# Optimization experiments

Measured on AMD Instinct MI355X. Metric: run time of the kernel, lower is better.

The kernel has to match this reference:

```python
import jax, jax.numpy as jnp
import numpy as np

W = 256  # window size


def _stack_neighbors(x):
    """x: (b, c, w, h, d) -> (b, c, w, h, d, 3): [prev chunk, self, next chunk],
    zero-padded at sequence boundaries (matches F.pad with value=0 in Longformer)."""
    prev = jnp.pad(x[:, :-1], ((0, 0), (1, 0), (0, 0), (0, 0), (0, 0)))
    nxt = jnp.pad(x[:, 1:], ((0, 0), (0, 1), (0, 0), (0, 0), (0, 0)))
    return jnp.stack([prev, x, nxt], axis=-1)


def setup_inputs() -> dict:
    key = jax.random.key(0)
    kq, kk, kv = jax.random.split(key, 3)
    b, s, h, d = 2, 8192, 8, 64
    return {
        "query": jax.random.normal(kq, (b, s, h, d), dtype=jnp.float32),
        "key": jax.random.normal(kk, (b, s, h, d), dtype=jnp.float32),
        "value": jax.random.normal(kv, (b, s, h, d), dtype=jnp.float32),
    }


def reference(query, key, value):
    b, s, h, d = query.shape
    c = s // W
    # --- sliding_chunks_no_overlap_matmul_qk ---
    chunk_q = query.reshape(b, c, W, h, d)
    chunk_k = key.reshape(b, c, W, h, d)
    k_exp = _stack_neighbors(chunk_k)            # (b, c, W, h, d, 3)
    # (b, c, W_q, h, 3, W_k)
    diag = jnp.einsum('bcxhd,bcyhde->bcxhey', chunk_q, k_exp)
    attention = diag.reshape(b, s, h, 3 * W)
    # softmax over the 3*W window positions (dropout = identity in eval)
    attention = jax.nn.softmax(attention, axis=-1)
    # --- sliding_chunks_no_overlap_matmul_pv ---
    chunk_prob = attention.reshape(b, c, W, h, 3, W)
    chunk_v = value.reshape(b, c, W, h, d)
    v_exp = _stack_neighbors(chunk_v)            # (b, c, W, h, d, 3)
    context = jnp.einsum('bcwhpd,bcdhep->bcwhe', chunk_prob, v_exp)
    output = context.reshape(b, s, h, d)
    return output, attention
```

## Files before the change

### kernel.cpp

```cpp
#include <hip/hip_runtime.h>


#define SEQ  8192
#define NH   8
#define DM   64
#define WIN  256
#define NC   32

typedef float  f32x4  __attribute__((ext_vector_type(4)));
typedef short  bf16x8 __attribute__((ext_vector_type(8)));
typedef short  bf16x4 __attribute__((ext_vector_type(4)));
typedef unsigned short u16;

__device__ __forceinline__ u16 bf16_rne(float x) {
    unsigned u = __builtin_bit_cast(unsigned, x);
    u += 0x7FFFu + ((u >> 16) & 1u);
    return (u16)(u >> 16);
}
__device__ __forceinline__ float bf16_f32(u16 h) {
    unsigned u = ((unsigned)h) << 16;
    return __builtin_bit_cast(float, u);
}

__global__ __launch_bounds__(256)
void wattn_prep(const float* __restrict__ kg, const float* __restrict__ vg,
                u16* __restrict__ khp, u16* __restrict__ klp, u16* __restrict__ vtp)
{
    __shared__ float tile[64 * 68];
    const int bid = blockIdx.x;
    const int t   = threadIdx.x;

    if (bid < 4096) {
        const size_t base = (size_t)bid * 2048 + t * 8;
        f32x4 a0 = *(const f32x4*)(kg + base);
        f32x4 a1 = *(const f32x4*)(kg + base + 4);
        bf16x8 h, l;
        #pragma unroll
        for (int i = 0; i < 8; ++i) {
            float f = (i < 4) ? a0[i] : a1[i - 4];
            u16 hh = bf16_rne(f);
            h[i] = (short)hh;
            l[i] = (short)bf16_rne(f - bf16_f32(hh));
        }
        *(bf16x8*)(khp + base) = h;
        *(bf16x8*)(klp + base) = l;
    } else {
        const int vid = bid - 4096;
        const int st  = vid & 127;
        const int hh  = (vid >> 7) & 7;
        const int bb  = vid >> 10;
        const int s0  = st * 64;

        const int r  = t >> 2;
        const int dg = (t & 3) * 16;
        const float* vp = vg + (((size_t)bb * SEQ + s0 + r) * NH + hh) * DM + dg;
        #pragma unroll
        for (int i = 0; i < 4; ++i)
            *(f32x4*)&tile[r * 68 + dg + 4 * i] = *(const f32x4*)(vp + 4 * i);
        __syncthreads();

        const int d  = t >> 2;
        const int sg = (t & 3) * 16;
        u16* op = vtp + (((size_t)bb * NH + hh) * DM + d) * SEQ + s0 + sg;
        bf16x8 o0, o1;
        #pragma unroll
        for (int j = 0; j < 8; ++j) o0[j] = (short)bf16_rne(tile[(sg + j) * 68 + d]);
        #pragma unroll
        for (int j = 0; j < 8; ++j) o1[j] = (short)bf16_rne(tile[(sg + 8 + j) * 68 + d]);
        *(bf16x8*)op       = o0;
        *(bf16x8*)(op + 8) = o1;
    }
}

__global__ __launch_bounds__(256, 2)
void wattn_mfma2(const float* __restrict__ qg, const u16* __restrict__ khp,
                 const u16* __restrict__ klp, const u16* __restrict__ vtp,
                 float* __restrict__ outg, float* __restrict__ attng)
{
    __shared__ __align__(16) char lds[35840];

    const int t    = threadIdx.x;
    const int lane = t & 63;
    const int w    = t >> 6;
    const int a    = lane & 15;
    const int g4   = lane >> 4;

    u16*   pw   = (u16*)(lds) + w * 2304;
    float* csc  = (float*)lds;
    float* smax = (float*)(lds + 34816);
    float* ssum = smax + 128;

    int gid = blockIdx.x;
    gid = (gid & 7) * 512 + (gid >> 3);
    const int tile = gid & 7;  gid >>= 3;
    const int hh   = gid & 7;  gid >>= 3;
    const int cc   = gid & 31; gid >>= 5;
    const int bb   = gid;
    const int row0 = cc * WIN + tile * 32;

    bf16x8 qh[2][2], ql[2][2];
    #pragma unroll
    for (int rt = 0; rt < 2; ++rt)
      #pragma unroll
      for (int ks = 0; ks < 2; ++ks) {
        const float* qp = qg + (((size_t)bb * SEQ + row0 + rt*16 + a) * NH + hh) * DM
                             + ks*32 + g4*8;
        f32x4 t0 = *(const f32x4*)qp;
        f32x4 t1 = *(const f32x4*)(qp + 4);
        #pragma unroll
        for (int i = 0; i < 8; ++i) {
            float f = (i < 4) ? t0[i] : t1[i - 4];
            u16 hv = bf16_rne(f);
            qh[rt][ks][i] = (short)hv;
            ql[rt][ks][i] = (short)bf16_rne(f - bf16_f32(hv));
        }
      }

    f32x4 acc[3][4][2];
    #pragma unroll
    for (int e = 0; e < 3; ++e)
      #pragma unroll
      for (int ct = 0; ct < 4; ++ct)
        #pragma unroll
        for (int rt = 0; rt < 2; ++rt)
            acc[e][ct][rt] = (f32x4){0.f, 0.f, 0.f, 0.f};

    #pragma unroll
    for (int e = 0; e < 3; ++e) {
        const int cs = cc + e - 1;
        if ((unsigned)cs < NC) {
            #pragma unroll
            for (int ct = 0; ct < 4; ++ct) {
                const size_t koff = (((size_t)bb * SEQ + cs*WIN + w*64 + ct*16 + a) * NH + hh) * DM
                                  + g4*8;
                #pragma unroll
                for (int ks = 0; ks < 2; ++ks) {
                    bf16x8 kh = *(const bf16x8*)(khp + koff + ks*32);
                    bf16x8 kl = *(const bf16x8*)(klp + koff + ks*32);
                    #pragma unroll
                    for (int rt = 0; rt < 2; ++rt) {
                        acc[e][ct][rt] = __builtin_amdgcn_mfma_f32_16x16x32_bf16(kh, qh[rt][ks], acc[e][ct][rt], 0, 0, 0);
                        acc[e][ct][rt] = __builtin_amdgcn_mfma_f32_16x16x32_bf16(kh, ql[rt][ks], acc[e][ct][rt], 0, 0, 0);
                        acc[e][ct][rt] = __builtin_amdgcn_mfma_f32_16x16x32_bf16(kl, qh[rt][ks], acc[e][ct][rt], 0, 0, 0);
                    }
                }
            }
        }
    }

    float M[2], INV[2];
    #pragma unroll
    for (int rt = 0; rt < 2; ++rt) {
        float mm = 0.f;
        #pragma unroll
        for (int e = 0; e < 3; ++e)
          #pragma unroll
          for (int ct = 0; ct < 4; ++ct)
            #pragma unroll
            for (int reg = 0; reg < 4; ++reg)
              mm = fmaxf(mm, acc[e][ct][rt][reg]);
        mm = fmaxf(mm, __shfl_xor(mm, 16));
        mm = fmaxf(mm, __shfl_xor(mm, 32));
        if (g4 == 0) smax[(rt*16 + a)*4 + w] = mm;
    }
    __syncthreads();
    #pragma unroll
    for (int rt = 0; rt < 2; ++rt) {
        const float* sp = smax + (rt*16 + a)*4;
        float mm = fmaxf(fmaxf(sp[0], sp[1]), fmaxf(sp[2], sp[3]));
        M[rt] = mm;
        float s = 0.f;
        #pragma unroll
        for (int e = 0; e < 3; ++e)
          #pragma unroll
          for (int ct = 0; ct < 4; ++ct)
            #pragma unroll
            for (int reg = 0; reg < 4; ++reg) {
                float p = __expf(acc[e][ct][rt][reg] - mm);
                acc[e][ct][rt][reg] = p;
                s += p;
            }
        s += __shfl_xor(s, 16);
        s += __shfl_xor(s, 32);
        if (g4 == 0) ssum[(rt*16 + a)*4 + w] = s;
    }
    __syncthreads();
    #pragma unroll
    for (int rt = 0; rt < 2; ++rt) {
        const float* sp = ssum + (rt*16 + a)*4;
        INV[rt] = 1.0f / (sp[0] + sp[1] + sp[2] + sp[3]);
    }

    #pragma unroll
    for (int rt = 0; rt < 2; ++rt) {
        float* ab = attng + (((size_t)bb * SEQ + row0 + rt*16 + a) * NH + hh) * 768
                          + w*64 + g4*4;
        #pragma unroll
        for (int e = 0; e < 3; ++e)
          #pragma unroll
          for (int ct = 0; ct < 4; ++ct) {
            f32x4 p = acc[e][ct][rt] * INV[rt];
            acc[e][ct][rt] = p;
            __builtin_nontemporal_store(p, (f32x4*)(ab + e*256 + ct*16));
          }
    }

    f32x4 acc2[4][2];
    #pragma unroll
    for (int dt = 0; dt < 4; ++dt)
      #pragma unroll
      for (int rt = 0; rt < 2; ++rt)
        acc2[dt][rt] = (f32x4){0.f, 0.f, 0.f, 0.f};

    #pragma unroll
    for (int e = 0; e < 3; ++e) {
        const int cs = cc + e - 1;
        if ((unsigned)cs < NC) {
            #pragma unroll
            for (int rt = 0; rt < 2; ++rt)
              #pragma unroll
              for (int ct = 0; ct < 4; ++ct) {
                f32x4 p = acc[e][ct][rt];
                bf16x4 pk;
                #pragma unroll
                for (int reg = 0; reg < 4; ++reg) pk[reg] = (short)bf16_rne(p[reg]);
                *(bf16x4*)(pw + (rt*16 + a)*72 + ct*16 + g4*4) = pk;
              }
            #pragma unroll
            for (int ks = 0; ks < 2; ++ks) {
                bf16x8 pb[2], va[4];
                #pragma unroll
                for (int rt = 0; rt < 2; ++rt)
                    pb[rt] = *(const bf16x8*)(pw + (rt*16 + a)*72 + ks*32 + g4*8);
                #pragma unroll
                for (int dt = 0; dt < 4; ++dt)
                    va[dt] = *(const bf16x8*)(vtp
                        + (((size_t)bb * NH + hh) * DM + dt*16 + a) * SEQ
                        + cs*WIN + w*64 + ks*32 + g4*8);
                #pragma unroll
                for (int dt = 0; dt < 4; ++dt)
                  #pragma unroll
                  for (int rt = 0; rt < 2; ++rt)
                    acc2[dt][rt] = __builtin_amdgcn_mfma_f32_16x16x32_bf16(va[dt], pb[rt], acc2[dt][rt], 0, 0, 0);
            }
        }
    }

    __syncthreads();
    #pragma unroll
    for (int dt = 0; dt < 4; ++dt)
      #pragma unroll
      for (int rt = 0; rt < 2; ++rt)
        *(f32x4*)&csc[w*2176 + (rt*16 + a)*68 + dt*16 + g4*4] = acc2[dt][rt];
    __syncthreads();
    #pragma unroll
    for (int r = 0; r < 8; ++r) {
        const int row = w*8 + r;
        float s = csc[          row*68 + lane] + csc[  2176 + row*68 + lane]
                + csc[2*2176 + row*68 + lane] + csc[3*2176 + row*68 + lane];
        __builtin_nontemporal_store(
            s, outg + (((size_t)bb * SEQ + row0 + row) * NH + hh) * DM + lane);
    }
}

__global__ __launch_bounds__(256, 2)
void wattn_mfma(const float* __restrict__ qg, const float* __restrict__ kg,
                const float* __restrict__ vg, float* __restrict__ outg,
                float* __restrict__ attng)
{
    __shared__ __align__(16) char lds[50176];
    const int t    = threadIdx.x;
    const int lane = t & 63;
    const int w    = t >> 6;
    const int a    = lane & 15;
    const int g4   = lane >> 4;

    unsigned short* vtw = (unsigned short*)(lds)         + w * 4096;
    unsigned short* plw = (unsigned short*)(lds + 32768) + w * 2048;
    float* smax = (float*)(lds + 49152);
    float* ssum = smax + 128;
    float* csc  = (float*)lds;

    int gid = blockIdx.x;
    gid = (gid & 7) * 512 + (gid >> 3);
    const int tile = gid & 7;  gid >>= 3;
    const int hh   = gid & 7;  gid >>= 3;
    const int cc   = gid & 31; gid >>= 5;
    const int bb   = gid;
    const int row0 = cc * WIN + tile * 32;

    bf16x8 qh[2][2], ql[2][2];
    #pragma unroll
    for (int rt = 0; rt < 2; ++rt)
      #pragma unroll
      for (int ks = 0; ks < 2; ++ks) {
        const float* qp = qg + (((size_t)bb * SEQ + row0 + rt*16 + a) * NH + hh) * DM
                             + ks*32 + g4*8;
        f32x4 t0 = *(const f32x4*)qp;
        f32x4 t1 = *(const f32x4*)(qp + 4);
        float f[8];
        #pragma unroll
        for (int i = 0; i < 4; ++i) { f[i] = t0[i]; f[4+i] = t1[i]; }
        #pragma unroll
        for (int i = 0; i < 8; ++i) {
            unsigned short h = bf16_rne(f[i]);
            qh[rt][ks][i] = (short)h;
            ql[rt][ks][i] = (short)bf16_rne(f[i] - bf16_f32(h));
        }
      }

    f32x4 acc[3][2][4];
    #pragma unroll
    for (int e = 0; e < 3; ++e)
      #pragma unroll
      for (int rt = 0; rt < 2; ++rt)
        #pragma unroll
        for (int ct = 0; ct < 4; ++ct)
            acc[e][rt][ct] = (f32x4){0.f, 0.f, 0.f, 0.f};

    #pragma unroll
    for (int e = 0; e < 3; ++e) {
        const int cs = cc + e - 1;
        if ((unsigned)cs < NC) {
            #pragma unroll
            for (int ct = 0; ct < 4; ++ct) {
                const float* kp = kg + (((size_t)bb * SEQ + cs*WIN + w*64 + ct*16 + a) * NH + hh) * DM;
                #pragma unroll
                for (int ks = 0; ks < 2; ++ks) {
                    f32x4 t0 = *(const f32x4*)(kp + ks*32 + g4*8);
                    f32x4 t1 = *(const f32x4*)(kp + ks*32 + g4*8 + 4);
                    float f[8];
                    #pragma unroll
                    for (int i = 0; i < 4; ++i) { f[i] = t0[i]; f[4+i] = t1[i]; }
                    bf16x8 kh, kl;
                    #pragma unroll
                    for (int i = 0; i < 8; ++i) {
                        unsigned short h = bf16_rne(f[i]);
                        kh[i] = (short)h;
                        kl[i] = (short)bf16_rne(f[i] - bf16_f32(h));
                    }
                    #pragma unroll
                    for (int rt = 0; rt < 2; ++rt) {
                        acc[e][rt][ct] = __builtin_amdgcn_mfma_f32_16x16x32_bf16(qh[rt][ks], kh, acc[e][rt][ct], 0, 0, 0);
                        acc[e][rt][ct] = __builtin_amdgcn_mfma_f32_16x16x32_bf16(qh[rt][ks], kl, acc[e][rt][ct], 0, 0, 0);
                        acc[e][rt][ct] = __builtin_amdgcn_mfma_f32_16x16x32_bf16(ql[rt][ks], kh, acc[e][rt][ct], 0, 0, 0);
                    }
                }
            }
        }
    }

    float M[2][4], INV[2][4];
    #pragma unroll
    for (int rt = 0; rt < 2; ++rt)
      #pragma unroll
      for (int reg = 0; reg < 4; ++reg) {
        float mm = -3.4e38f;
        #pragma unroll
        for (int e = 0; e < 3; ++e)
          #pragma unroll
          for (int ct = 0; ct < 4; ++ct)
            mm = fmaxf(mm, acc[e][rt][ct][reg]);
        mm = fmaxf(mm, __shfl_xor(mm, 1));
        mm = fmaxf(mm, __shfl_xor(mm, 2));
        mm = fmaxf(mm, __shfl_xor(mm, 4));
        mm = fmaxf(mm, __shfl_xor(mm, 8));
        if (a == 0) smax[(rt*16 + g4*4 + reg)*4 + w] = mm;
      }
    __syncthreads();
    #pragma unroll
    for (int rt = 0; rt < 2; ++rt)
      #pragma unroll
      for (int reg = 0; reg < 4; ++reg) {
        const float* sp = smax + (rt*16 + g4*4 + reg)*4;
        float mm = fmaxf(fmaxf(sp[0], sp[1]), fmaxf(sp[2], sp[3]));
        M[rt][reg] = mm;
        float s = 0.f;
        #pragma unroll
        for (int e = 0; e < 3; ++e)
          #pragma unroll
          for (int ct = 0; ct < 4; ++ct) {
            float p = __expf(acc[e][rt][ct][reg] - mm);
            acc[e][rt][ct][reg] = p;
            s += p;
          }
        s += __shfl_xor(s, 1);
        s += __shfl_xor(s, 2);
        s += __shfl_xor(s, 4);
        s += __shfl_xor(s, 8);
        if (a == 0) ssum[(rt*16 + g4*4 + reg)*4 + w] = s;
      }
    __syncthreads();
    #pragma unroll
    for (int rt = 0; rt < 2; ++rt)
      #pragma unroll
      for (int reg = 0; reg < 4; ++reg) {
        const float* sp = ssum + (rt*16 + g4*4 + reg)*4;
        INV[rt][reg] = 1.0f / (sp[0] + sp[1] + sp[2] + sp[3]);
      }

    #pragma unroll
    for (int rt = 0; rt < 2; ++rt)
      #pragma unroll
      for (int reg = 0; reg < 4; ++reg) {
        const float iv = INV[rt][reg];
        float* ab = attng + (((size_t)bb * SEQ + row0 + rt*16 + g4*4 + reg) * NH + hh) * 768
                          + w*64 + a;
        #pragma unroll
        for (int e = 0; e < 3; ++e)
          #pragma unroll
          for (int ct = 0; ct < 4; ++ct) {
            float p = acc[e][rt][ct][reg] * iv;
            acc[e][rt][ct][reg] = p;
            __builtin_nontemporal_store(p, ab + e*256 + ct*16);
          }
      }

    f32x4 acc2[2][4];
    #pragma unroll
    for (int rt = 0; rt < 2; ++rt)
      #pragma unroll
      for (int dt = 0; dt < 4; ++dt)
        acc2[rt][dt] = (f32x4){0.f, 0.f, 0.f, 0.f};

    #pragma unroll
    for (int e = 0; e < 3; ++e) {
        const int cs = cc + e - 1;
        if ((unsigned)cs < NC) {
            __syncthreads();
            #pragma unroll
            for (int i = 0; i < 16; ++i) {
                const int kk = i*4 + g4;
                const float* vp = vg + (((size_t)bb * SEQ + cs*WIN + w*64 + kk) * NH + hh) * DM
                                     + a*4;
                f32x4 v4 = *(const f32x4*)vp;
                #pragma unroll
                for (int j = 0; j < 4; ++j) {
                    const int d = a*4 + j;
                    vtw[(d>>4)*1024 + (kk>>3)*128 + (d&15)*8 + (kk&7)] = bf16_rne(v4[j]);
                }
            }
            #pragma unroll
            for (int rt = 0; rt < 2; ++rt)
              #pragma unroll
              for (int reg = 0; reg < 4; ++reg) {
                const int prow = rt*16 + g4*4 + reg;
                #pragma unroll
                for (int ct = 0; ct < 4; ++ct) {
                    const int key = ct*16 + a;
                    plw[prow*64 + (((key>>3) ^ (prow&7)) << 3) + (key&7)] =
                        bf16_rne(acc[e][rt][ct][reg]);
                }
              }
            __syncthreads();
            #pragma unroll
            for (int ks = 0; ks < 2; ++ks) {
                bf16x8 pa[2], vb[4];
                #pragma unroll
                for (int rt = 0; rt < 2; ++rt) {
                    const int prow = rt*16 + a;
                    pa[rt] = *(const bf16x8*)(plw + prow*64 + ((((ks<<2) + g4) ^ (prow&7)) << 3));
                }
                #pragma unroll
                for (int dt = 0; dt < 4; ++dt)
                    vb[dt] = *(const bf16x8*)(vtw + dt*1024 + ((ks<<2) + g4)*128 + a*8);
                #pragma unroll
                for (int rt = 0; rt < 2; ++rt)
                  #pragma unroll
                  for (int dt = 0; dt < 4; ++dt)
                    acc2[rt][dt] = __builtin_amdgcn_mfma_f32_16x16x32_bf16(pa[rt], vb[dt], acc2[rt][dt], 0, 0, 0);
            }
        }
    }

    __syncthreads();
    #pragma unroll
    for (int rt = 0; rt < 2; ++rt)
      #pragma unroll
      for (int dt = 0; dt < 4; ++dt)
        #pragma unroll
        for (int reg = 0; reg < 4; ++reg)
          csc[w*2176 + (rt*16 + g4*4 + reg)*68 + dt*16 + a] = acc2[rt][dt][reg];
    __syncthreads();
    #pragma unroll
    for (int r = 0; r < 8; ++r) {
        const int row = w*8 + r;
        float s = csc[          row*68 + lane] + csc[  2176 + row*68 + lane]
                + csc[2*2176 + row*68 + lane] + csc[3*2176 + row*68 + lane];
        __builtin_nontemporal_store(
            s, outg + (((size_t)bb * SEQ + row0 + row) * NH + hh) * DM + lane);
    }
}

extern "C" void kernel_launch(void* const* d_in, const int* in_sizes, int n_in,
                              void* d_out, int out_size, void* d_ws, size_t ws_size,
                              hipStream_t stream) {
    const float* q = (const float*)d_in[0];
    const float* k = (const float*)d_in[1];
    const float* v = (const float*)d_in[2];

    float* out  = (float*)d_out;
    float* attn = (float*)d_out + (size_t)2 * SEQ * NH * DM;

    const size_t NELEM = (size_t)2 * SEQ * NH * DM;
    const size_t NEED  = 3 * NELEM * sizeof(u16);

    if (ws_size >= NEED) {
        u16* khp = (u16*)d_ws;
        u16* klp = khp + NELEM;
        u16* vtp = klp + NELEM;
        wattn_prep<<<dim3(6144), dim3(256), 0, stream>>>(k, v, khp, klp, vtp);
        wattn_mfma2<<<dim3(4096), dim3(256), 0, stream>>>(q, khp, klp, vtp, out, attn);
    } else {
        wattn_mfma<<<dim3(4096), dim3(256), 0, stream>>>(q, k, v, out, attn);
    }
}
```

Measured before the change: 638.8 us.

## Relayout K and V workspaces per head and raise occupancy to four blocks

The prep kernel now writes the bf16 hi/lo K split in a (b,h,s,d) layout and V transposed into per-64-token tiles, so each head's keys and values are contiguous. The main kernel's K and V address math is updated to match, which makes its global reads more contiguous. Launch bounds go from 2 to 4 blocks per CU to raise occupancy, at the risk of register spills given the large accumulator arrays. Unused max arrays are also removed.

```diff
diff --git a/kernel.cpp b/kernel.cpp
--- a/kernel.cpp
+++ b/kernel.cpp
@@ -31,25 +31,33 @@
     const int t   = threadIdx.x;
 
     if (bid < 4096) {
-        const size_t base = (size_t)bid * 2048 + t * 8;
-        f32x4 a0 = *(const f32x4*)(kg + base);
-        f32x4 a1 = *(const f32x4*)(kg + base + 4);
+        int id = bid;
+        const int sp = id & 255; id >>= 8;
+        const int hh = id & 7;   id >>= 3;
+        const int bb = id;
+        const int r  = t >> 3;
+        const int c  = (t & 7) * 8;
+        const int s0 = sp * 32;
+        const float* ip = kg + (((size_t)bb * SEQ + s0 + r) * NH + hh) * DM + c;
+        f32x4 a0 = *(const f32x4*)ip;
+        f32x4 a1 = *(const f32x4*)(ip + 4);
         bf16x8 h, l;
         #pragma unroll
         for (int i = 0; i < 8; ++i) {
             float f = (i < 4) ? a0[i] : a1[i - 4];
-            u16 hh = bf16_rne(f);
-            h[i] = (short)hh;
-            l[i] = (short)bf16_rne(f - bf16_f32(hh));
-        }
-        *(bf16x8*)(khp + base) = h;
-        *(bf16x8*)(klp + base) = l;
+            u16 hv = bf16_rne(f);
+            h[i] = (short)hv;
+            l[i] = (short)bf16_rne(f - bf16_f32(hv));
+        }
+        const size_t ooff = (((size_t)bb * NH + hh) * SEQ + s0 + r) * DM + c;
+        *(bf16x8*)(khp + ooff) = h;
+        *(bf16x8*)(klp + ooff) = l;
     } else {
-        const int vid = bid - 4096;
-        const int st  = vid & 127;
-        const int hh  = (vid >> 7) & 7;
-        const int bb  = vid >> 10;
-        const int s0  = st * 64;
+        int vid = bid - 4096;
+        const int p  = vid & 127; vid >>= 7;
+        const int hh = vid & 7;   vid >>= 3;
+        const int bb = vid;
+        const int s0 = p * 64;
 
         const int r  = t >> 2;
         const int dg = (t & 3) * 16;
@@ -61,7 +69,7 @@
 
         const int d  = t >> 2;
         const int sg = (t & 3) * 16;
-        u16* op = vtp + (((size_t)bb * NH + hh) * DM + d) * SEQ + s0 + sg;
+        u16* op = vtp + ((((size_t)bb * NH + hh) * 128 + p) * DM + d) * 64 + sg;
         bf16x8 o0, o1;
         #pragma unroll
         for (int j = 0; j < 8; ++j) o0[j] = (short)bf16_rne(tile[(sg + j) * 68 + d]);
@@ -72,8 +80,8 @@
     }
 }
 
-__global__ __launch_bounds__(256, 2)
-void wattn_mfma2(const float* __restrict__ qg, const u16* __restrict__ khp,
+__global__ __launch_bounds__(256, 4)
+void wattn_mfma3(const float* __restrict__ qg, const u16* __restrict__ khp,
                  const u16* __restrict__ klp, const u16* __restrict__ vtp,
                  float* __restrict__ outg, float* __restrict__ attng)
 {
@@ -131,7 +139,7 @@
         if ((unsigned)cs < NC) {
             #pragma unroll
             for (int ct = 0; ct < 4; ++ct) {
-                const size_t koff = (((size_t)bb * SEQ + cs*WIN + w*64 + ct*16 + a) * NH + hh) * DM
+                const size_t koff = (((size_t)bb * NH + hh) * SEQ + cs*WIN + w*64 + ct*16 + a) * DM
                                   + g4*8;
                 #pragma unroll
                 for (int ks = 0; ks < 2; ++ks) {
@@ -148,7 +156,7 @@
         }
     }
 
-    float M[2], INV[2];
+    float INV[2];
     #pragma unroll
     for (int rt = 0; rt < 2; ++rt) {
         float mm = 0.f;
@@ -168,7 +176,6 @@
     for (int rt = 0; rt < 2; ++rt) {
         const float* sp = smax + (rt*16 + a)*4;
         float mm = fmaxf(fmaxf(sp[0], sp[1]), fmaxf(sp[2], sp[3]));
-        M[rt] = mm;
         float s = 0.f;
         #pragma unroll
         for (int e = 0; e < 3; ++e)
@@ -235,8 +242,8 @@
                 #pragma unroll
                 for (int dt = 0; dt < 4; ++dt)
                     va[dt] = *(const bf16x8*)(vtp
-                        + (((size_t)bb * NH + hh) * DM + dt*16 + a) * SEQ
-                        + cs*WIN + w*64 + ks*32 + g4*8);
+                        + ((((size_t)bb * NH + hh) * 128 + cs*4 + w) * DM + dt*16 + a) * 64
+                        + ks*32 + g4*8);
                 #pragma unroll
                 for (int dt = 0; dt < 4; ++dt)
                   #pragma unroll
@@ -350,7 +357,7 @@
         }
     }
 
-    float M[2][4], INV[2][4];
+    float INV[2][4];
     #pragma unroll
     for (int rt = 0; rt < 2; ++rt)
       #pragma unroll
@@ -374,7 +381,6 @@
       for (int reg = 0; reg < 4; ++reg) {
         const float* sp = smax + (rt*16 + g4*4 + reg)*4;
         float mm = fmaxf(fmaxf(sp[0], sp[1]), fmaxf(sp[2], sp[3]));
-        M[rt][reg] = mm;
         float s = 0.f;
         #pragma unroll
         for (int e = 0; e < 3; ++e)
@@ -510,7 +516,7 @@
         u16* klp = khp + NELEM;
         u16* vtp = klp + NELEM;
         wattn_prep<<<dim3(6144), dim3(256), 0, stream>>>(k, v, khp, klp, vtp);
-        wattn_mfma2<<<dim3(4096), dim3(256), 0, stream>>>(q, khp, klp, vtp, out, attn);
+        wattn_mfma3<<<dim3(4096), dim3(256), 0, stream>>>(q, khp, klp, vtp, out, attn);
     } else {
         wattn_mfma<<<dim3(4096), dim3(256), 0, stream>>>(q, k, v, out, attn);
     }
```

After: 685.0 us. 1.07x slower.
